# Kernel tuning notes

Measured on AMD Instinct MI355X. Metric: run time of the kernel, lower is better.

The kernel has to match this reference:

```python
import jax, jax.numpy as jnp
import numpy as np

B, T, D = 128, 256, 1024

def setup_inputs() -> dict:
    key = jax.random.key(0)
    ks = jax.random.split(key, 7)
    s = 1.0 / np.sqrt(D)
    return {
        "inputs": jax.random.normal(ks[0], (B, T, D), dtype=jnp.float32),
        "Wk": jax.random.uniform(ks[1], (D, D), jnp.float32, -s, s),
        "bk": jax.random.uniform(ks[2], (D,), jnp.float32, -s, s),
        "Wq": jax.random.uniform(ks[3], (D, D), jnp.float32, -s, s),
        "bq": jax.random.uniform(ks[4], (D,), jnp.float32, -s, s),
        "Wv": jax.random.uniform(ks[5], (D, D), jnp.float32, -s, s),
        "bv": jax.random.uniform(ks[6], (D,), jnp.float32, -s, s),
    }

def reference(inputs, Wk, bk, Wq, bq, Wv, bv):
    # torch.nn.Linear: y = x @ W.T + b
    keys = inputs @ Wk.T + bk        # [B, T, D]
    queries = inputs @ Wq.T + bq     # [B, T, D]
    values = inputs @ Wv.T + bv      # [B, T, D]
    scale = 1.0 / jnp.sqrt(jnp.float32(inputs.shape[-1]))
    scores = jnp.einsum('btd,bsd->bts', queries, keys) * scale  # [B, T, T]
    t = inputs.shape[1]
    causal = jnp.tril(jnp.ones((t, t), dtype=bool))
    scores = jnp.where(causal, scores, -jnp.inf)
    probs = jax.nn.softmax(scores, axis=-1)
    return jnp.einsum('bts,bsd->btd', probs, values)
```

## Files before the change

kernel.cpp:

```cpp
#include <hip/hip_runtime.h>
#include <hip/hip_bf16.h>


typedef __attribute__((ext_vector_type(4))) float f32x4;
typedef __attribute__((ext_vector_type(8))) short s16x8;
typedef unsigned short u16;

__device__ inline u16 f2bf(float f) {
    union { __hip_bfloat16 h; u16 u; } c;
    c.h = __float2bfloat16(f);
    return c.u;
}

__global__ __launch_bounds__(256) void cvt_f32_bf16(const float* __restrict__ in,
                                                    u16* __restrict__ out, int n4) {
    int stride = gridDim.x * blockDim.x;
    for (int i = blockIdx.x * blockDim.x + threadIdx.x; i < n4; i += stride) {
        float4 v = reinterpret_cast<const float4*>(in)[i];
        ushort4 o = make_ushort4(f2bf(v.x), f2bf(v.y), f2bf(v.z), f2bf(v.w));
        reinterpret_cast<ushort4*>(out)[i] = o;
    }
}

__device__ inline void gemm_mainloop(const u16* __restrict__ Ap, const u16* __restrict__ Bp,
                                     int lda, int ldb, int kLen,
                                     u16* As, u16* Bs, f32x4 (&acc)[4][4]) {
    const int tid  = threadIdx.x;
    const int lane = tid & 63;
    const int wr   = (tid >> 7) & 1;
    const int wc   = (tid >> 6) & 1;
    const int sr   = tid >> 3;
    const int sc   = (tid & 7) << 3;

    for (int k0 = 0; k0 < kLen; k0 += 64) {
#pragma unroll
        for (int it = 0; it < 4; ++it) {
            int r = it * 32 + sr;
            *reinterpret_cast<s16x8*>(&As[r * 64 + sc]) =
                *reinterpret_cast<const s16x8*>(&Ap[(size_t)r * lda + k0 + sc]);
            *reinterpret_cast<s16x8*>(&Bs[r * 64 + sc]) =
                *reinterpret_cast<const s16x8*>(&Bp[(size_t)r * ldb + k0 + sc]);
        }
        __syncthreads();
#pragma unroll
        for (int kk = 0; kk < 64; kk += 32) {
            const int kcol = kk + (lane >> 4) * 8;
            s16x8 a[4], bfr[4];
#pragma unroll
            for (int m = 0; m < 4; ++m)
                a[m] = *reinterpret_cast<const s16x8*>(&As[(wr * 64 + m * 16 + (lane & 15)) * 64 + kcol]);
#pragma unroll
            for (int n = 0; n < 4; ++n)
                bfr[n] = *reinterpret_cast<const s16x8*>(&Bs[(wc * 64 + n * 16 + (lane & 15)) * 64 + kcol]);
#pragma unroll
            for (int m = 0; m < 4; ++m)
#pragma unroll
                for (int n = 0; n < 4; ++n)
                    acc[m][n] = __builtin_amdgcn_mfma_f32_16x16x32_bf16(a[m], bfr[n], acc[m][n], 0, 0, 0);
        }
        __syncthreads();
    }
}

__global__ __launch_bounds__(256) void qkv_gemm(const u16* __restrict__ X, const u16* __restrict__ W3,
                                                const float* __restrict__ biasK,
                                                const float* __restrict__ biasQ,
                                                const float* __restrict__ biasV,
                                                u16* __restrict__ Kb, u16* __restrict__ Qb,
                                                u16* __restrict__ Vt) {
    __shared__ u16 As[128 * 64];
    __shared__ u16 Bs[128 * 64];
    const int bid  = blockIdx.x;
    const int nt   = bid % 24;
    const int mt   = bid / 24;
    const int nmat = nt >> 3;
    const int ncol = nt & 7;
    const u16* Ap = X + (size_t)mt * 128 * 1024;
    const u16* Bp = W3 + (size_t)nmat * 1024 * 1024 + (size_t)ncol * 128 * 1024;

    f32x4 acc[4][4] = {};
    gemm_mainloop(Ap, Bp, 1024, 1024, 1024, As, Bs, acc);

    const int tid  = threadIdx.x;
    const int lane = tid & 63;
    const int wr   = (tid >> 7) & 1;
    const int wc   = (tid >> 6) & 1;
    const float* bias = (nmat == 0) ? biasK : (nmat == 1) ? biasQ : biasV;
    u16* outKQ = (nmat == 0) ? Kb : Qb;
    const int r0 = (lane >> 4) << 2;
    const int c0 = lane & 15;
#pragma unroll
    for (int m = 0; m < 4; ++m) {
#pragma unroll
        for (int n = 0; n < 4; ++n) {
            const int colg = ncol * 128 + wc * 64 + n * 16 + c0;
            const float bvv = bias[colg];
#pragma unroll
            for (int j = 0; j < 4; ++j) {
                const int rowg = mt * 128 + wr * 64 + m * 16 + r0 + j;
                const u16 hb = f2bf(acc[m][n][j] + bvv);
                if (nmat == 2) {
                    const int b = rowg >> 8, t = rowg & 255;
                    Vt[(size_t)b * 262144 + (size_t)colg * 256 + t] = hb;
                } else {
                    outKQ[(size_t)rowg * 1024 + colg] = hb;
                }
            }
        }
    }
}

__global__ __launch_bounds__(256) void scores_gemm(const u16* __restrict__ Qb,
                                                   const u16* __restrict__ Kb,
                                                   float* __restrict__ S) {
    __shared__ u16 As[128 * 64];
    __shared__ u16 Bs[128 * 64];
    const int bid = blockIdx.x;
    const int b   = bid / 3;
    const int rem = bid % 3;
    const int ti  = (rem == 0) ? 0 : 1;
    const int si  = (rem == 2) ? 1 : 0;
    const u16* Ap = Qb + ((size_t)b * 256 + (size_t)ti * 128) * 1024;
    const u16* Bp = Kb + ((size_t)b * 256 + (size_t)si * 128) * 1024;

    f32x4 acc[4][4] = {};
    gemm_mainloop(Ap, Bp, 1024, 1024, 1024, As, Bs, acc);

    const int tid  = threadIdx.x;
    const int lane = tid & 63;
    const int wr   = (tid >> 7) & 1;
    const int wc   = (tid >> 6) & 1;
    const int r0 = (lane >> 4) << 2;
    const int c0 = lane & 15;
    const float scale = 0.03125f;
#pragma unroll
    for (int m = 0; m < 4; ++m) {
#pragma unroll
        for (int n = 0; n < 4; ++n) {
            const int s = si * 128 + wc * 64 + n * 16 + c0;
#pragma unroll
            for (int j = 0; j < 4; ++j) {
                const int t = ti * 128 + wr * 64 + m * 16 + r0 + j;
                float v = acc[m][n][j] * scale;
                if (s > t) v = -__builtin_inff();
                S[(size_t)b * 65536 + (size_t)t * 256 + s] = v;
            }
        }
    }
}

__global__ __launch_bounds__(256) void softmax_p(const float* __restrict__ S, u16* __restrict__ P) {
    const int row  = blockIdx.x * 4 + (threadIdx.x >> 6);
    const int lane = threadIdx.x & 63;
    const int b = row >> 8, t = row & 255;
    const float* Sp = S + (size_t)b * 65536 + (size_t)t * 256;
    const int s0 = lane * 4;
    float4 v = reinterpret_cast<const float4*>(Sp)[lane];
    const float NEG = -__builtin_inff();
    float x0 = (s0 + 0 <= t) ? v.x : NEG;
    float x1 = (s0 + 1 <= t) ? v.y : NEG;
    float x2 = (s0 + 2 <= t) ? v.z : NEG;
    float x3 = (s0 + 3 <= t) ? v.w : NEG;
    float mx = fmaxf(fmaxf(x0, x1), fmaxf(x2, x3));
#pragma unroll
    for (int off = 1; off < 64; off <<= 1) mx = fmaxf(mx, __shfl_xor(mx, off, 64));
    float e0 = (s0 + 0 <= t) ? __expf(x0 - mx) : 0.f;
    float e1 = (s0 + 1 <= t) ? __expf(x1 - mx) : 0.f;
    float e2 = (s0 + 2 <= t) ? __expf(x2 - mx) : 0.f;
    float e3 = (s0 + 3 <= t) ? __expf(x3 - mx) : 0.f;
    float sum = e0 + e1 + e2 + e3;
#pragma unroll
    for (int off = 1; off < 64; off <<= 1) sum += __shfl_xor(sum, off, 64);
    const float inv = 1.0f / sum;
    ushort4 o = make_ushort4(f2bf(e0 * inv), f2bf(e1 * inv), f2bf(e2 * inv), f2bf(e3 * inv));
    reinterpret_cast<ushort4*>(P + (size_t)row * 256)[lane] = o;
}

__global__ __launch_bounds__(256) void pv_gemm(const u16* __restrict__ P, const u16* __restrict__ Vt,
                                               float* __restrict__ O) {
    __shared__ u16 As[128 * 64];
    __shared__ u16 Bs[128 * 64];
    const int bid = blockIdx.x;
    const int b   = bid >> 4;
    const int r   = bid & 15;
    const int mt  = r >> 3;
    const int ntl = r & 7;
    const u16* Ap = P + (size_t)b * 65536 + (size_t)mt * 128 * 256;
    const u16* Bp = Vt + (size_t)b * 262144 + (size_t)ntl * 128 * 256;
    const int kmax = (mt + 1) * 128;

    f32x4 acc[4][4] = {};
    gemm_mainloop(Ap, Bp, 256, 256, kmax, As, Bs, acc);

    const int tid  = threadIdx.x;
    const int lane = tid & 63;
    const int wr   = (tid >> 7) & 1;
    const int wc   = (tid >> 6) & 1;
    const int r0 = (lane >> 4) << 2;
    const int c0 = lane & 15;
#pragma unroll
    for (int m = 0; m < 4; ++m) {
#pragma unroll
        for (int n = 0; n < 4; ++n) {
            const int d = ntl * 128 + wc * 64 + n * 16 + c0;
#pragma unroll
            for (int j = 0; j < 4; ++j) {
                const int t = mt * 128 + wr * 64 + m * 16 + r0 + j;
                O[((size_t)b * 256 + t) * 1024 + d] = acc[m][n][j];
            }
        }
    }
}

extern "C" void kernel_launch(void* const* d_in, const int* in_sizes, int n_in,
                              void* d_out, int out_size, void* d_ws, size_t ws_size,
                              hipStream_t stream) {
    (void)in_sizes; (void)n_in; (void)out_size; (void)ws_size;
    const float* x  = (const float*)d_in[0];
    const float* Wk = (const float*)d_in[1];
    const float* bk = (const float*)d_in[2];
    const float* Wq = (const float*)d_in[3];
    const float* bq = (const float*)d_in[4];
    const float* Wv = (const float*)d_in[5];
    const float* bv = (const float*)d_in[6];
    float* out = (float*)d_out;
    char* ws = (char*)d_ws;

    u16*   xb = (u16*)(ws + 0);
    u16*   Wb = (u16*)(ws + 67108864);
    u16*   Kb = (u16*)(ws + 73400320);
    u16*   Qb = (u16*)(ws + 140509184);
    u16*   Vt = (u16*)(ws + 207618048);
    float* S  = (float*)(ws + 0);
    u16*   P  = (u16*)(ws + 33554432);

    cvt_f32_bf16<<<2048, 256, 0, stream>>>(x, xb, 33554432 / 4);
    cvt_f32_bf16<<<512, 256, 0, stream>>>(Wk, Wb, 1048576 / 4);
    cvt_f32_bf16<<<512, 256, 0, stream>>>(Wq, Wb + 1048576, 1048576 / 4);
    cvt_f32_bf16<<<512, 256, 0, stream>>>(Wv, Wb + 2097152, 1048576 / 4);
    qkv_gemm<<<6144, 256, 0, stream>>>(xb, Wb, bk, bq, bv, Kb, Qb, Vt);
    scores_gemm<<<384, 256, 0, stream>>>(Qb, Kb, S);
    softmax_p<<<8192, 256, 0, stream>>>(S, P);
    pv_gemm<<<2048, 256, 0, stream>>>(P, Vt, out);
}
```

Measured before the change: 483.4 us.

## Replace QKV GEMM with 256x256-tile, 8-wave kernel using direct-to-LDS double buffering

Replaces the 128x128 QKV projection GEMM with a 256x256 tile kernel of 512 threads. It stages tiles straight from global memory into swizzled, double-buffered LDS via global_load_lds and splits each k-step into four MFMA phases interleaved with the next tile's loads. It also uses block-index swizzling for L2 locality and raises wave priority around MFMA bursts. The aim is to cut global traffic per FLOP and hide load latency, at the cost of 128KB dynamic LDS, low occupancy, and many barriers.

```diff
diff --git a/kernel.cpp b/kernel.cpp
--- a/kernel.cpp
+++ b/kernel.cpp
@@ -11,6 +11,16 @@
     c.h = __float2bfloat16(f);
     return c.u;
 }
+
+__device__ __forceinline__ void stage16(const void* g, void* l) {
+    __builtin_amdgcn_global_load_lds((const __attribute__((address_space(1))) void*)g,
+                                     (__attribute__((address_space(3))) void*)l, 16, 0, 0);
+}
+
+#define FENCE() asm volatile("" ::: "memory")
+#define BAR() do { FENCE(); __builtin_amdgcn_s_barrier(); \
+                   __builtin_amdgcn_sched_barrier(0); FENCE(); } while (0)
+#define MFMA(a_, b_, c_) (c_) = __builtin_amdgcn_mfma_f32_16x16x32_bf16((a_), (b_), (c_), 0, 0, 0)
 
 __global__ __launch_bounds__(256) void cvt_f32_bf16(const float* __restrict__ in,
                                                     u16* __restrict__ out, int n4) {
@@ -19,6 +29,162 @@
         float4 v = reinterpret_cast<const float4*>(in)[i];
         ushort4 o = make_ushort4(f2bf(v.x), f2bf(v.y), f2bf(v.z), f2bf(v.w));
         reinterpret_cast<ushort4*>(out)[i] = o;
+    }
+}
+
+__global__ __launch_bounds__(512, 2) void qkv256(const u16* __restrict__ X, const u16* __restrict__ W3,
+                                                 const float* __restrict__ biasK,
+                                                 const float* __restrict__ biasQ,
+                                                 const float* __restrict__ biasV,
+                                                 u16* __restrict__ Kb, u16* __restrict__ Qb,
+                                                 u16* __restrict__ Vt) {
+    extern __shared__ char lds[];
+
+    const int bid = blockIdx.x;
+    const int swz = (bid & 7) * 192 + (bid >> 3);
+    const int mt = swz / 12, nt2 = swz % 12;
+    const int nmat = nt2 >> 2, ncol = nt2 & 3;
+    const u16* Asrc = X + (size_t)mt * 256 * 1024;
+    const u16* Bsrc = W3 + (size_t)nmat * 1048576 + (size_t)ncol * 256 * 1024;
+
+    const int tid  = threadIdx.x;
+    const int lane = tid & 63, w = tid >> 6;
+    const int wr = w >> 2, wc = w & 3;
+    const int l15 = lane & 15, l16 = lane >> 4;
+    const int sw0 = ((0 + l16) ^ (l15 & 7)) << 4;
+    const int sw1 = ((4 + l16) ^ (l15 & 7)) << 4;
+    const int lr = lane >> 3, ls = lane & 7;
+    const int stg_col = (ls ^ lr) << 3;
+
+    auto STG = [&](const u16* srcHalf, int colbase, char* dstHalf) {
+        const u16* s0 = srcHalf + (size_t)(w * 16 + lr) * 1024 + colbase + stg_col;
+        stage16(s0,            dstHalf + w * 2048);
+        stage16(s0 + 8 * 1024, dstHalf + w * 2048 + 1024);
+    };
+
+    f32x4 acc[8][4] = {};
+    s16x8 af[4][2], bf[4][2];
+
+    STG(Asrc,              0, lds + 0);
+    STG(Asrc + 128 * 1024, 0, lds + 16384);
+    STG(Bsrc,              0, lds + 32768);
+    STG(Bsrc + 128 * 1024, 0, lds + 49152);
+    STG(Asrc,             64, lds + 65536 + 0);
+    asm volatile("s_waitcnt vmcnt(2)" ::: "memory");
+    BAR();
+
+    for (int t = 0; t < 16; ++t) {
+        char* bufc = lds + (t & 1) * 65536;
+        char* bufn = lds + ((t + 1) & 1) * 65536;
+        const char* Ah = bufc + wr * 16384;
+        const char* Bh = bufc + 32768 + (wc >> 1) * 16384;
+        const int brow = (wc & 1) * 64;
+        const int nk = (t + 1) * 64;
+
+#pragma unroll
+        for (int fm = 0; fm < 4; ++fm) {
+            const int r = fm * 16 + l15;
+            af[fm][0] = *(const s16x8*)(Ah + r * 128 + sw0);
+            af[fm][1] = *(const s16x8*)(Ah + r * 128 + sw1);
+        }
+#pragma unroll
+        for (int fn = 0; fn < 2; ++fn) {
+            const int r = brow + fn * 16 + l15;
+            bf[fn][0] = *(const s16x8*)(Bh + r * 128 + sw0);
+            bf[fn][1] = *(const s16x8*)(Bh + r * 128 + sw1);
+        }
+        if (t < 15) STG(Asrc + 128 * 1024, nk, bufn + 16384);
+        BAR();
+        __builtin_amdgcn_s_setprio(1);
+#pragma unroll
+        for (int fm = 0; fm < 4; ++fm)
+#pragma unroll
+            for (int fn = 0; fn < 2; ++fn) {
+                MFMA(af[fm][0], bf[fn][0], acc[fm][fn]);
+                MFMA(af[fm][1], bf[fn][1], acc[fm][fn]);
+            }
+        __builtin_amdgcn_s_setprio(0);
+        BAR();
+
+#pragma unroll
+        for (int fn = 2; fn < 4; ++fn) {
+            const int r = brow + fn * 16 + l15;
+            bf[fn][0] = *(const s16x8*)(Bh + r * 128 + sw0);
+            bf[fn][1] = *(const s16x8*)(Bh + r * 128 + sw1);
+        }
+        if (t < 15) STG(Bsrc, nk, bufn + 32768);
+        BAR();
+        __builtin_amdgcn_s_setprio(1);
+#pragma unroll
+        for (int fm = 0; fm < 4; ++fm)
+#pragma unroll
+            for (int fn = 2; fn < 4; ++fn) {
+                MFMA(af[fm][0], bf[fn][0], acc[fm][fn]);
+                MFMA(af[fm][1], bf[fn][1], acc[fm][fn]);
+            }
+        __builtin_amdgcn_s_setprio(0);
+        BAR();
+
+#pragma unroll
+        for (int fm = 0; fm < 4; ++fm) {
+            const int r = 64 + fm * 16 + l15;
+            af[fm][0] = *(const s16x8*)(Ah + r * 128 + sw0);
+            af[fm][1] = *(const s16x8*)(Ah + r * 128 + sw1);
+        }
+        if (t < 15) STG(Bsrc + 128 * 1024, nk, bufn + 49152);
+        BAR();
+        __builtin_amdgcn_s_setprio(1);
+#pragma unroll
+        for (int fm = 0; fm < 4; ++fm)
+#pragma unroll
+            for (int fn = 0; fn < 2; ++fn) {
+                MFMA(af[fm][0], bf[fn][0], acc[fm + 4][fn]);
+                MFMA(af[fm][1], bf[fn][1], acc[fm + 4][fn]);
+            }
+        __builtin_amdgcn_s_setprio(0);
+        BAR();
+
+        if (t < 14) {
+            STG(Asrc, (t + 2) * 64, bufc + 0);
+            asm volatile("s_waitcnt vmcnt(2)" ::: "memory");
+        } else if (t == 14) {
+            asm volatile("s_waitcnt vmcnt(0)" ::: "memory");
+        }
+        BAR();
+        __builtin_amdgcn_s_setprio(1);
+#pragma unroll
+        for (int fm = 0; fm < 4; ++fm)
+#pragma unroll
+            for (int fn = 2; fn < 4; ++fn) {
+                MFMA(af[fm][0], bf[fn][0], acc[fm + 4][fn]);
+                MFMA(af[fm][1], bf[fn][1], acc[fm + 4][fn]);
+            }
+        __builtin_amdgcn_s_setprio(0);
+        BAR();
+    }
+
+    const float* bias = (nmat == 0) ? biasK : (nmat == 1) ? biasQ : biasV;
+    u16* outKQ = (nmat == 0) ? Kb : Qb;
+    const int colbase = ncol * 256 + wc * 64;
+#pragma unroll
+    for (int FM = 0; FM < 8; ++FM) {
+#pragma unroll
+        for (int fn = 0; fn < 4; ++fn) {
+            const int col = colbase + fn * 16 + l15;
+            const float bvv = bias[col];
+            const int rbase = mt * 256 + wr * 128 + FM * 16 + (l16 << 2);
+#pragma unroll
+            for (int j = 0; j < 4; ++j) {
+                const int row = rbase + j;
+                const u16 hb = f2bf(acc[FM][fn][j] + bvv);
+                if (nmat == 2) {
+                    const int b = row >> 8, tt = row & 255;
+                    Vt[(size_t)b * 262144 + (size_t)col * 256 + tt] = hb;
+                } else {
+                    outKQ[(size_t)row * 1024 + col] = hb;
+                }
+            }
+        }
     }
 }
 
@@ -59,54 +225,6 @@
                     acc[m][n] = __builtin_amdgcn_mfma_f32_16x16x32_bf16(a[m], bfr[n], acc[m][n], 0, 0, 0);
         }
         __syncthreads();
-    }
-}
-
-__global__ __launch_bounds__(256) void qkv_gemm(const u16* __restrict__ X, const u16* __restrict__ W3,
-                                                const float* __restrict__ biasK,
-                                                const float* __restrict__ biasQ,
-                                                const float* __restrict__ biasV,
-                                                u16* __restrict__ Kb, u16* __restrict__ Qb,
-                                                u16* __restrict__ Vt) {
-    __shared__ u16 As[128 * 64];
-    __shared__ u16 Bs[128 * 64];
-    const int bid  = blockIdx.x;
-    const int nt   = bid % 24;
-    const int mt   = bid / 24;
-    const int nmat = nt >> 3;
-    const int ncol = nt & 7;
-    const u16* Ap = X + (size_t)mt * 128 * 1024;
-    const u16* Bp = W3 + (size_t)nmat * 1024 * 1024 + (size_t)ncol * 128 * 1024;
-
-    f32x4 acc[4][4] = {};
-    gemm_mainloop(Ap, Bp, 1024, 1024, 1024, As, Bs, acc);
-
-    const int tid  = threadIdx.x;
-    const int lane = tid & 63;
-    const int wr   = (tid >> 7) & 1;
-    const int wc   = (tid >> 6) & 1;
-    const float* bias = (nmat == 0) ? biasK : (nmat == 1) ? biasQ : biasV;
-    u16* outKQ = (nmat == 0) ? Kb : Qb;
-    const int r0 = (lane >> 4) << 2;
-    const int c0 = lane & 15;
-#pragma unroll
-    for (int m = 0; m < 4; ++m) {
-#pragma unroll
-        for (int n = 0; n < 4; ++n) {
-            const int colg = ncol * 128 + wc * 64 + n * 16 + c0;
-            const float bvv = bias[colg];
-#pragma unroll
-            for (int j = 0; j < 4; ++j) {
-                const int rowg = mt * 128 + wr * 64 + m * 16 + r0 + j;
-                const u16 hb = f2bf(acc[m][n][j] + bvv);
-                if (nmat == 2) {
-                    const int b = rowg >> 8, t = rowg & 255;
-                    Vt[(size_t)b * 262144 + (size_t)colg * 256 + t] = hb;
-                } else {
-                    outKQ[(size_t)rowg * 1024 + colg] = hb;
-                }
-            }
-        }
     }
 }
 
@@ -238,7 +356,7 @@
     cvt_f32_bf16<<<512, 256, 0, stream>>>(Wk, Wb, 1048576 / 4);
     cvt_f32_bf16<<<512, 256, 0, stream>>>(Wq, Wb + 1048576, 1048576 / 4);
     cvt_f32_bf16<<<512, 256, 0, stream>>>(Wv, Wb + 2097152, 1048576 / 4);
-    qkv_gemm<<<6144, 256, 0, stream>>>(xb, Wb, bk, bq, bv, Kb, Qb, Vt);
+    qkv256<<<1536, 512, 131072, stream>>>(xb, Wb, bk, bq, bv, Kb, Qb, Vt);
     scores_gemm<<<384, 256, 0, stream>>>(Qb, Kb, S);
     softmax_p<<<8192, 256, 0, stream>>>(S, P);
     pv_gemm<<<2048, 256, 0, stream>>>(P, Vt, out);
```

Result: faster. 424.1 us (-12.3%).

## Replace QKV GEMM with 256x256-tile pipelined kernel using direct global-to-LDS loads

Applied to the files above, without the earlier changes.

The QKV projection GEMM is rewritten with 256x256 output tiles, 512 threads, and a 4-stage LDS ring buffer filled by global_load_lds. Loads run ahead with vmcnt-based waits so memory traffic overlaps the MFMA work. The kernel also adds XOR-swizzled LDS layout, double-buffered register fragments, s_setprio around MFMA bursts, and block-index swizzling for L2 locality. The goal is to cut global re-reads and sync stalls of the old 128x128 synchronous kernel, at the cost of 128KB dynamic LDS per block, higher register pressure, and fragile hand-tuned waitcnt logic.

```diff
diff --git a/kernel.cpp b/kernel.cpp
--- a/kernel.cpp
+++ b/kernel.cpp
@@ -11,6 +11,13 @@
     c.h = __float2bfloat16(f);
     return c.u;
 }
+
+__device__ __forceinline__ void stage16(const void* g, void* l) {
+    __builtin_amdgcn_global_load_lds((const __attribute__((address_space(1))) void*)g,
+                                     (__attribute__((address_space(3))) void*)l, 16, 0, 0);
+}
+
+#define MFMA(a_, b_, c_) (c_) = __builtin_amdgcn_mfma_f32_16x16x32_bf16((a_), (b_), (c_), 0, 0, 0)
 
 __global__ __launch_bounds__(256) void cvt_f32_bf16(const float* __restrict__ in,
                                                     u16* __restrict__ out, int n4) {
@@ -19,6 +26,122 @@
         float4 v = reinterpret_cast<const float4*>(in)[i];
         ushort4 o = make_ushort4(f2bf(v.x), f2bf(v.y), f2bf(v.z), f2bf(v.w));
         reinterpret_cast<ushort4*>(out)[i] = o;
+    }
+}
+
+__global__ __launch_bounds__(512, 2) void qkv256(const u16* __restrict__ X, const u16* __restrict__ W3,
+                                                 const float* __restrict__ biasK,
+                                                 const float* __restrict__ biasQ,
+                                                 const float* __restrict__ biasV,
+                                                 u16* __restrict__ Kb, u16* __restrict__ Qb,
+                                                 u16* __restrict__ Vt) {
+    extern __shared__ char lds[];
+
+    const int bid = blockIdx.x;
+    const int swz = (bid & 7) * 192 + (bid >> 3);
+    const int mt = swz / 12, nt2 = swz % 12;
+    const int nmat = nt2 >> 2, ncol = nt2 & 3;
+    const u16* Asrc = X + (size_t)mt * 256 * 1024;
+    const u16* Bsrc = W3 + (size_t)nmat * 1048576 + (size_t)ncol * 256 * 1024;
+
+    const int tid  = threadIdx.x;
+    const int lane = tid & 63, w = tid >> 6;
+    const int wr = w >> 2, wc = w & 3;
+    const int l15 = lane & 15, l16 = lane >> 4;
+
+    const int lds_ro = l15 * 64 + ((l16 ^ ((l15 >> 1) & 3)) << 4);
+    const int aoff = wr * 128 * 64 + lds_ro;
+    const int boff = 16384 + wc * 64 * 64 + lds_ro;
+
+    const int isB = w >> 2;
+    const u16* dsrc = isB ? Bsrc : Asrc;
+    const int drow  = (w & 3) * 64 + (lane >> 2);
+    const int dslot = ((lane & 3) ^ ((lane >> 3) & 3)) * 8;
+    const u16* dptr0 = dsrc + (size_t)drow * 1024 + dslot;
+    const int dlds = isB * 16384 + (w & 3) * 4096;
+
+#define STAGE(u_) do {                                                            \
+        char* bb_ = lds + (((u_) & 3) * 32768) + dlds;                            \
+        const u16* gp_ = dptr0 + (size_t)(u_) * 32;                               \
+        stage16(gp_,             bb_);                                            \
+        stage16(gp_ + 16 * 1024, bb_ + 1024);                                     \
+        stage16(gp_ + 32 * 1024, bb_ + 2048);                                     \
+        stage16(gp_ + 48 * 1024, bb_ + 3072);                                     \
+    } while (0)
+
+#define READS(u_, a_, b_) do {                                                    \
+        const char* bp_ = lds + (((u_) & 3) * 32768);                             \
+        _Pragma("unroll")                                                         \
+        for (int fm = 0; fm < 8; ++fm)                                            \
+            a_[fm] = *(const s16x8*)(bp_ + aoff + fm * 1024);                     \
+        _Pragma("unroll")                                                         \
+        for (int fn = 0; fn < 4; ++fn)                                            \
+            b_[fn] = *(const s16x8*)(bp_ + boff + fn * 1024);                     \
+    } while (0)
+
+#define MFMAS(a_, b_) do {                                                        \
+        __builtin_amdgcn_s_setprio(1);                                            \
+        _Pragma("unroll")                                                         \
+        for (int fm = 0; fm < 8; ++fm)                                            \
+            _Pragma("unroll")                                                     \
+            for (int fn = 0; fn < 4; ++fn)                                        \
+                MFMA(a_[fm], b_[fn], acc[fm][fn]);                                \
+        __builtin_amdgcn_s_setprio(0);                                            \
+    } while (0)
+
+    f32x4 acc[8][4] = {};
+    s16x8 a0[8], b0[4], a1[8], b1[4];
+
+    STAGE(0); STAGE(1); STAGE(2);
+    asm volatile("s_waitcnt vmcnt(4)" ::: "memory");
+    __builtin_amdgcn_s_barrier();
+    READS(0, a0, b0);
+
+    for (int tt = 0; tt < 15; ++tt) {
+        const int u1 = 2 * tt + 1, u2 = 2 * tt + 2;
+        if (u1 + 2 <= 31) STAGE(u1 + 2);
+        READS(u1, a1, b1);
+        MFMAS(a0, b0);
+        if (u1 <= 29) asm volatile("s_waitcnt vmcnt(4)" ::: "memory");
+        else          asm volatile("s_waitcnt vmcnt(0)" ::: "memory");
+        __builtin_amdgcn_s_barrier();
+        if (u2 + 2 <= 31) STAGE(u2 + 2);
+        READS(u2, a0, b0);
+        MFMAS(a1, b1);
+        if (u2 <= 29) asm volatile("s_waitcnt vmcnt(4)" ::: "memory");
+        else          asm volatile("s_waitcnt vmcnt(0)" ::: "memory");
+        __builtin_amdgcn_s_barrier();
+    }
+    READS(31, a1, b1);
+    MFMAS(a0, b0);
+    MFMAS(a1, b1);
+
+#undef STAGE
+#undef READS
+#undef MFMAS
+
+    const float* bias = (nmat == 0) ? biasK : (nmat == 1) ? biasQ : biasV;
+    u16* outKQ = (nmat == 0) ? Kb : Qb;
+    const int colbase = ncol * 256 + wc * 64;
+#pragma unroll
+    for (int FM = 0; FM < 8; ++FM) {
+#pragma unroll
+        for (int fn = 0; fn < 4; ++fn) {
+            const int col = colbase + fn * 16 + l15;
+            const float bvv = bias[col];
+            const int rbase = mt * 256 + wr * 128 + FM * 16 + (l16 << 2);
+#pragma unroll
+            for (int j = 0; j < 4; ++j) {
+                const int row = rbase + j;
+                const u16 hb = f2bf(acc[FM][fn][j] + bvv);
+                if (nmat == 2) {
+                    const int b = row >> 8, tt2 = row & 255;
+                    Vt[(size_t)b * 262144 + (size_t)col * 256 + tt2] = hb;
+                } else {
+                    outKQ[(size_t)row * 1024 + col] = hb;
+                }
+            }
+        }
     }
 }
 
@@ -59,54 +182,6 @@
                     acc[m][n] = __builtin_amdgcn_mfma_f32_16x16x32_bf16(a[m], bfr[n], acc[m][n], 0, 0, 0);
         }
         __syncthreads();
-    }
-}
-
-__global__ __launch_bounds__(256) void qkv_gemm(const u16* __restrict__ X, const u16* __restrict__ W3,
-                                                const float* __restrict__ biasK,
-                                                const float* __restrict__ biasQ,
-                                                const float* __restrict__ biasV,
-                                                u16* __restrict__ Kb, u16* __restrict__ Qb,
-                                                u16* __restrict__ Vt) {
-    __shared__ u16 As[128 * 64];
-    __shared__ u16 Bs[128 * 64];
-    const int bid  = blockIdx.x;
-    const int nt   = bid % 24;
-    const int mt   = bid / 24;
-    const int nmat = nt >> 3;
-    const int ncol = nt & 7;
-    const u16* Ap = X + (size_t)mt * 128 * 1024;
-    const u16* Bp = W3 + (size_t)nmat * 1024 * 1024 + (size_t)ncol * 128 * 1024;
-
-    f32x4 acc[4][4] = {};
-    gemm_mainloop(Ap, Bp, 1024, 1024, 1024, As, Bs, acc);
-
-    const int tid  = threadIdx.x;
-    const int lane = tid & 63;
-    const int wr   = (tid >> 7) & 1;
-    const int wc   = (tid >> 6) & 1;
-    const float* bias = (nmat == 0) ? biasK : (nmat == 1) ? biasQ : biasV;
-    u16* outKQ = (nmat == 0) ? Kb : Qb;
-    const int r0 = (lane >> 4) << 2;
-    const int c0 = lane & 15;
-#pragma unroll
-    for (int m = 0; m < 4; ++m) {
-#pragma unroll
-        for (int n = 0; n < 4; ++n) {
-            const int colg = ncol * 128 + wc * 64 + n * 16 + c0;
-            const float bvv = bias[colg];
-#pragma unroll
-            for (int j = 0; j < 4; ++j) {
-                const int rowg = mt * 128 + wr * 64 + m * 16 + r0 + j;
-                const u16 hb = f2bf(acc[m][n][j] + bvv);
-                if (nmat == 2) {
-                    const int b = rowg >> 8, t = rowg & 255;
-                    Vt[(size_t)b * 262144 + (size_t)colg * 256 + t] = hb;
-                } else {
-                    outKQ[(size_t)rowg * 1024 + colg] = hb;
-                }
-            }
-        }
     }
 }
 
@@ -238,7 +313,7 @@
     cvt_f32_bf16<<<512, 256, 0, stream>>>(Wk, Wb, 1048576 / 4);
     cvt_f32_bf16<<<512, 256, 0, stream>>>(Wq, Wb + 1048576, 1048576 / 4);
     cvt_f32_bf16<<<512, 256, 0, stream>>>(Wv, Wb + 2097152, 1048576 / 4);
-    qkv_gemm<<<6144, 256, 0, stream>>>(xb, Wb, bk, bq, bv, Kb, Qb, Vt);
+    qkv256<<<1536, 512, 131072, stream>>>(xb, Wb, bk, bq, bv, Kb, Qb, Vt);
     scores_gemm<<<384, 256, 0, stream>>>(Qb, Kb, S);
     softmax_p<<<8192, 256, 0, stream>>>(S, P);
     pv_gemm<<<2048, 256, 0, stream>>>(P, Vt, out);
```

After: 417.8 us. 13.6% less time.

## Rewrite QKV GEMM with direct-to-LDS double-buffered loads and 128x256 tiles

Applied to the files above, without the earlier changes.

Replaces the QKV projection GEMM with a 512-thread kernel that computes 128x256 output tiles. It uses global_load_lds to stage 32-wide K slices directly into a swizzled, double-buffered LDS layout, so the next slice loads while MFMAs run on the current one. The kernel also adds block-index swizzling for cache locality and s_setprio around the MFMA burst. This is meant to hide global-load latency and cut LDS bank conflicts and register staging, at the cost of a more intricate loop with a barrier on every 32-wide K step.

```diff
diff --git a/kernel.cpp b/kernel.cpp
--- a/kernel.cpp
+++ b/kernel.cpp
@@ -11,6 +11,13 @@
     c.h = __float2bfloat16(f);
     return c.u;
 }
+
+__device__ __forceinline__ void stage16(const void* g, void* l) {
+    __builtin_amdgcn_global_load_lds((const __attribute__((address_space(1))) void*)g,
+                                     (__attribute__((address_space(3))) void*)l, 16, 0, 0);
+}
+
+#define MFMA(a_, b_, c_) (c_) = __builtin_amdgcn_mfma_f32_16x16x32_bf16((a_), (b_), (c_), 0, 0, 0)
 
 __global__ __launch_bounds__(256) void cvt_f32_bf16(const float* __restrict__ in,
                                                     u16* __restrict__ out, int n4) {
@@ -22,6 +29,95 @@
     }
 }
 
+__global__ __launch_bounds__(512, 4) void qkv128(const u16* __restrict__ X, const u16* __restrict__ W3,
+                                                 const float* __restrict__ biasK,
+                                                 const float* __restrict__ biasQ,
+                                                 const float* __restrict__ biasV,
+                                                 u16* __restrict__ Kb, u16* __restrict__ Qb,
+                                                 u16* __restrict__ Vt) {
+    __shared__ char lds[49152];
+
+    const int bid = blockIdx.x;
+    const int swz = (bid & 7) * 384 + (bid >> 3);
+    const int mt = swz / 12, nt2 = swz % 12;
+    const int nmat = nt2 >> 2, ncol = nt2 & 3;
+    const u16* Asrc = X + (size_t)mt * 128 * 1024;
+    const u16* Bsrc = W3 + (size_t)nmat * 1048576 + (size_t)ncol * 256 * 1024;
+
+    const int tid  = threadIdx.x;
+    const int lane = tid & 63, w = tid >> 6;
+    const int wr = w >> 2, wc = w & 3;
+    const int l15 = lane & 15, l16 = lane >> 4;
+
+    const int rdoff = l15 * 64 + (((l16 ^ ((l15 >> 1) & 3)) & 3) << 4);
+    const int aoff = wr * 4096 + rdoff;
+    const int boff = 8192 + wc * 4096 + rdoff;
+
+    const int srow = tid >> 2, sslot = tid & 3;
+    const int scol = (sslot ^ ((srow >> 1) & 3)) * 8;
+    const u16* asrcp  = Asrc + (size_t)srow * 1024 + scol;
+    const u16* bsrcp0 = Bsrc + (size_t)srow * 1024 + scol;
+    const u16* bsrcp1 = Bsrc + (size_t)(srow + 128) * 1024 + scol;
+
+    f32x4 acc[4][4] = {};
+
+#define STG(u_) do {                                                              \
+        char* bb_ = lds + (((u_) & 1) * 24576) + w * 1024;                        \
+        const size_t ko_ = (size_t)(u_) * 32;                                     \
+        stage16(asrcp  + ko_, bb_);                                               \
+        stage16(bsrcp0 + ko_, bb_ + 8192);                                        \
+        stage16(bsrcp1 + ko_, bb_ + 16384);                                       \
+    } while (0)
+
+    STG(0);
+    asm volatile("s_waitcnt vmcnt(0)" ::: "memory");
+    __builtin_amdgcn_s_barrier();
+
+    for (int u = 0; u < 32; ++u) {
+        if (u < 31) STG(u + 1);
+        const char* bp = lds + (u & 1) * 24576;
+        s16x8 a[4], b[4];
+#pragma unroll
+        for (int fm = 0; fm < 4; ++fm) a[fm] = *(const s16x8*)(bp + aoff + fm * 1024);
+#pragma unroll
+        for (int fn = 0; fn < 4; ++fn) b[fn] = *(const s16x8*)(bp + boff + fn * 1024);
+        __builtin_amdgcn_s_setprio(1);
+#pragma unroll
+        for (int fm = 0; fm < 4; ++fm)
+#pragma unroll
+            for (int fn = 0; fn < 4; ++fn)
+                MFMA(a[fm], b[fn], acc[fm][fn]);
+        __builtin_amdgcn_s_setprio(0);
+        asm volatile("s_waitcnt vmcnt(0)" ::: "memory");
+        __builtin_amdgcn_s_barrier();
+    }
+#undef STG
+
+    const float* bias = (nmat == 0) ? biasK : (nmat == 1) ? biasQ : biasV;
+    u16* outKQ = (nmat == 0) ? Kb : Qb;
+    const int r0 = l16 << 2;
+#pragma unroll
+    for (int m = 0; m < 4; ++m) {
+#pragma unroll
+        for (int n = 0; n < 4; ++n) {
+            const int col = ncol * 256 + wc * 64 + n * 16 + l15;
+            const float bvv = bias[col];
+            const int rbase = mt * 128 + wr * 64 + m * 16 + r0;
+#pragma unroll
+            for (int j = 0; j < 4; ++j) {
+                const int row = rbase + j;
+                const u16 hb = f2bf(acc[m][n][j] + bvv);
+                if (nmat == 2) {
+                    const int b2 = row >> 8, tt2 = row & 255;
+                    Vt[(size_t)b2 * 262144 + (size_t)col * 256 + tt2] = hb;
+                } else {
+                    outKQ[(size_t)row * 1024 + col] = hb;
+                }
+            }
+        }
+    }
+}
+
 __device__ inline void gemm_mainloop(const u16* __restrict__ Ap, const u16* __restrict__ Bp,
                                      int lda, int ldb, int kLen,
                                      u16* As, u16* Bs, f32x4 (&acc)[4][4]) {
@@ -59,54 +155,6 @@
                     acc[m][n] = __builtin_amdgcn_mfma_f32_16x16x32_bf16(a[m], bfr[n], acc[m][n], 0, 0, 0);
         }
         __syncthreads();
-    }
-}
-
-__global__ __launch_bounds__(256) void qkv_gemm(const u16* __restrict__ X, const u16* __restrict__ W3,
-                                                const float* __restrict__ biasK,
-                                                const float* __restrict__ biasQ,
-                                                const float* __restrict__ biasV,
-                                                u16* __restrict__ Kb, u16* __restrict__ Qb,
-                                                u16* __restrict__ Vt) {
-    __shared__ u16 As[128 * 64];
-    __shared__ u16 Bs[128 * 64];
-    const int bid  = blockIdx.x;
-    const int nt   = bid % 24;
-    const int mt   = bid / 24;
-    const int nmat = nt >> 3;
-    const int ncol = nt & 7;
-    const u16* Ap = X + (size_t)mt * 128 * 1024;
-    const u16* Bp = W3 + (size_t)nmat * 1024 * 1024 + (size_t)ncol * 128 * 1024;
-
-    f32x4 acc[4][4] = {};
-    gemm_mainloop(Ap, Bp, 1024, 1024, 1024, As, Bs, acc);
-
-    const int tid  = threadIdx.x;
-    const int lane = tid & 63;
-    const int wr   = (tid >> 7) & 1;
-    const int wc   = (tid >> 6) & 1;
-    const float* bias = (nmat == 0) ? biasK : (nmat == 1) ? biasQ : biasV;
-    u16* outKQ = (nmat == 0) ? Kb : Qb;
-    const int r0 = (lane >> 4) << 2;
-    const int c0 = lane & 15;
-#pragma unroll
-    for (int m = 0; m < 4; ++m) {
-#pragma unroll
-        for (int n = 0; n < 4; ++n) {
-            const int colg = ncol * 128 + wc * 64 + n * 16 + c0;
-            const float bvv = bias[colg];
-#pragma unroll
-            for (int j = 0; j < 4; ++j) {
-                const int rowg = mt * 128 + wr * 64 + m * 16 + r0 + j;
-                const u16 hb = f2bf(acc[m][n][j] + bvv);
-                if (nmat == 2) {
-                    const int b = rowg >> 8, t = rowg & 255;
-                    Vt[(size_t)b * 262144 + (size_t)colg * 256 + t] = hb;
-                } else {
-                    outKQ[(size_t)rowg * 1024 + colg] = hb;
-                }
-            }
-        }
     }
 }
 
@@ -238,7 +286,7 @@
     cvt_f32_bf16<<<512, 256, 0, stream>>>(Wk, Wb, 1048576 / 4);
     cvt_f32_bf16<<<512, 256, 0, stream>>>(Wq, Wb + 1048576, 1048576 / 4);
     cvt_f32_bf16<<<512, 256, 0, stream>>>(Wv, Wb + 2097152, 1048576 / 4);
-    qkv_gemm<<<6144, 256, 0, stream>>>(xb, Wb, bk, bq, bv, Kb, Qb, Vt);
+    qkv128<<<3072, 512, 0, stream>>>(xb, Wb, bk, bq, bv, Kb, Qb, Vt);
     scores_gemm<<<384, 256, 0, stream>>>(Qb, Kb, S);
     softmax_p<<<8192, 256, 0, stream>>>(S, P);
     pv_gemm<<<2048, 256, 0, stream>>>(P, Vt, out);
```

After: 425.1 us. 1.14x faster.
